# Kernel tuning notes

Measured on AMD Instinct MI355X. Metric: run time of the kernel, lower is better.

## Reference

```python
import jax, jax.numpy as jnp
import numpy as np
import math

# ---- constants lifted verbatim from the torch source ----
PMLX = 10; PX = 400; TX = PMLX + PX + PMLX          # txsize = 420
PMLY = 10; PY = 400; TY = PMLY + PY + PMLY          # tysize = 420
CX = TX // 2; CY = TY // 2
EPS0 = 1e-9 / 36 / math.pi
MU0 = 4 * math.pi * 1e-7
C0 = 1.0 / math.sqrt(MU0 * EPS0)
DX = 2.5e-8; DY = 2.5e-8
DT = 0.99 / C0 / math.sqrt((1.0 / DX) ** 2 + (1.0 / DY) ** 2)
EPSR_INF = 5.283
EPS_INF = EPS0 * EPSR_INF
F0 = 5.47e14; BW = 0.1 * F0
T = math.sqrt(2.0) * math.sqrt(math.log(2.0)) / (math.pi * BW)
NSTEPS = 200   # reduced from 16000 for the correctness baseline; same per-step math


def setup_inputs() -> dict:
    # Lorentz (complex-pole) silver model from param(): pole/residue -> a0,a1,b0,b1,b2
    pr, pi_ = -4.8113e12, 6.8512e13
    rr, ri = 4.9581e14, -1.511e18
    a0 = -2.0 * (pr * rr + pi_ * ri)
    a1 = 2.0 * rr
    b0 = pr * pr + pi_ * pi_
    b1 = -2.0 * pr
    b2 = 1.0
    den = b0 * DT * DT + 2 * b1 * DT + 4 * b2
    Ca = np.array([-(2 * b0 * DT * DT - 8 * b2) / den], np.float32)
    Cb = np.array([-(b0 * DT * DT - 2 * b1 * DT + 4 * b2) / den], np.float32)
    Cc = np.array([(2 * a0 * EPS0 * DT + 4 * a1 * EPS0) / den], np.float32)
    Cd = np.array([-(8 * a1 * EPS0) / den], np.float32)
    Ce = np.array([(-2 * a0 * EPS0 * DT + 4 * a1 * EPS0) / den], np.float32)
    temp1 = float(Cc[0])                       # sum over tot_pol = 1 pole
    denom = EPS_INF / DT + 0.5 * temp1
    C1 = np.full((TX + 1, TY + 1), (EPS_INF / DT) / denom, np.float32)
    C2 = np.full((TX + 1, TY + 1), 0.5 / denom, np.float32)
    Cb_dx = np.full((TX + 1, TY + 1), 1.0 / denom / DX, np.float32)
    Cb_dy = np.full((TX + 1, TY + 1), 1.0 / denom / DY, np.float32)
    dbhx = np.full((TX + 1, TY), DT / MU0 / DY, np.float32)   # Hx curl coeff
    dbhy = np.full((TX, TY + 1), DT / MU0 / DX, np.float32)   # Hy curl coeff
    # polynomial-graded PML conductivity profiles (pml_param)
    m = 4
    eta0 = 120.0 * math.pi
    smax = 0.8 * (m + 1) / (eta0 * DX)

    def prof(n, npml, off):
        k = np.arange(n, dtype=np.float64)
        dl = np.clip(npml - k - off, 0.0, None) / npml   # depth into left PML
        dr = np.clip(k + off - (n - 1 - npml), 0.0, None) / npml
        return (smax * (dl ** m + dr ** m)).astype(np.float32)

    sig_ex = prof(TX + 1, PMLX, 0.0)
    sig_ey = prof(TY + 1, PMLY, 0.0)
    sig_hx = prof(TX, PMLX, 0.5)   # H nodes on half-grid
    sig_hy = prof(TY, PMLY, 0.5)
    # Gaussian-modulated sine soft source at the grid center
    t = np.arange(NSTEPS, dtype=np.float64) * DT
    src = (np.exp(-(((t - 4 * T) / T) ** 2)) * np.sin(2 * math.pi * F0 * (t - 4 * T))).astype(np.float32)
    return {
        "src": jnp.asarray(src), "C1": jnp.asarray(C1), "C2": jnp.asarray(C2),
        "Cb_dx": jnp.asarray(Cb_dx), "Cb_dy": jnp.asarray(Cb_dy),
        "dbhx": jnp.asarray(dbhx), "dbhy": jnp.asarray(dbhy),
        "Ca": jnp.asarray(Ca), "Cb": jnp.asarray(Cb), "Cc": jnp.asarray(Cc),
        "Cd": jnp.asarray(Cd), "Ce": jnp.asarray(Ce),
        "sig_ex": jnp.asarray(sig_ex), "sig_ey": jnp.asarray(sig_ey),
        "sig_hx": jnp.asarray(sig_hx), "sig_hy": jnp.asarray(sig_hy),
        "n_steps": NSTEPS,
    }


def reference(src, C1, C2, Cb_dx, Cb_dy, dbhx, dbhy, Ca, Cb, Cc, Cd, Ce,
              sig_ex, sig_ey, sig_hx, sig_hy, n_steps):
    # PML damping factors (exponential time-stepping of the conductive loss)
    de = jnp.exp(-(sig_ex[:, None] + sig_ey[None, :]) * (DT / EPS0))     # (421,421) for Ez
    dhx = jnp.exp(-(sig_ex[:, None] + sig_hy[None, :]) * (DT / MU0))     # (421,420) for Hx
    dhy = jnp.exp(-(sig_hx[:, None] + sig_ey[None, :]) * (DT / MU0))     # (420,421) for Hy
    # PEC outer boundary mask
    mask = jnp.pad(jnp.ones((TX - 1, TY - 1), de.dtype), ((1, 1), (1, 1)))
    ca = Ca[:, None, None]; cb = Cb[:, None, None]; cc = Cc[:, None, None]
    cd = Cd[:, None, None]; ce = Ce[:, None, None]

    def step(carry, s):
        Ez, Eold, Hx, Hy, Jz, Jold = carry
        # H-field Yee updates with PML damping
        Hx = dhx * (Hx - dbhx * (Ez[:, 1:] - Ez[:, :-1]))
        Hy = dhy * (Hy + dbhy * (Ez[1:, :] - Ez[:-1, :]))
        # curls onto Ez nodes (interior), zero-padded at PEC boundary
        curlHy = jnp.pad(Hy[1:, :] - Hy[:-1, :], ((1, 1), (0, 0)))       # (421,421)
        curlHx = jnp.pad(Hx[:, 1:] - Hx[:, :-1], ((0, 0), (1, 1)))       # (421,421)
        # Lorentz ADE dispersion source term (tot_pol summed; Cc*Ez^{n+1} folded into C1/C2/Cb_*)
        Phi = jnp.sum((ca + 1.0) * Jz + cb * Jold + cd * Ez[None] + ce * Eold[None], axis=0)
        Ez_new = mask * de * (C1 * Ez + Cb_dx * curlHy - Cb_dy * curlHx - C2 * Phi)
        Ez_new = Ez_new.at[CX, CY].add(s)                                 # soft point source
        # polarization current recurrence
        Jz_new = ca * Jz + cb * Jold + cc * Ez_new[None] + cd * Ez[None] + ce * Eold[None]
        return (Ez_new, Ez, Hx, Hy, Jz_new, Jz), None

    z = jnp.zeros((TX + 1, TY + 1), src.dtype)
    init = (z, z,
            jnp.zeros((TX + 1, TY), src.dtype),
            jnp.zeros((TX, TY + 1), src.dtype),
            jnp.zeros((1, TX + 1, TY + 1), src.dtype),
            jnp.zeros((1, TX + 1, TY + 1), src.dtype))
    (Ez, _, _, _, _, _), _ = jax.lax.scan(step, init, src[:n_steps])
    return Ez
```

## Files before the change

### kernel.cpp

```cpp
#include <hip/hip_runtime.h>
#include <math.h>

#define NXr 421
#define CXr 210
#define NSTEPS_C 200

#define Bt   16
#define Kt   8
#define EXT  32
#define SPITCH 34
#define NBLK 27
#define NPHASE (NSTEPS_C / Kt)

#define PP   448
#define PAD  8
#define CP   (CXr + PAD)
#define FSZ  (PP * PP)

struct PParams {
    float *aEz, *aEo, *aJz, *aJo, *aHx, *aHy;
    float *bEz, *bEo, *bJz, *bJo, *bHx, *bHy;
    const float *dexP, *deyP, *aexP, *aeyP, *ahxP, *ahyP;
    const float *C1a, *C2a, *Cbdxa, *Cbdya;
    const float *Caa, *Cba, *Cca, *Cda, *Cea, *dbhxa, *dbhya;
    const float *src;
};

__global__ void init_kernel(const float* __restrict__ sig_ex,
                            const float* __restrict__ sig_ey,
                            const float* __restrict__ sig_hx,
                            const float* __restrict__ sig_hy,
                            float de_fac, float dh_fac,
                            float* __restrict__ zero_base, int n_zero,
                            float* __restrict__ dexP, float* __restrict__ deyP,
                            float* __restrict__ aexP, float* __restrict__ aeyP,
                            float* __restrict__ ahxP, float* __restrict__ ahyP)
{
    int t = blockIdx.x * blockDim.x + threadIdx.x;
    int stride = gridDim.x * blockDim.x;
    for (int k = t; k < n_zero; k += stride) zero_base[k] = 0.0f;
    if (t < PP) {
        int g = t - PAD;
        dexP[t] = (g >= 1 && g <= NXr - 2) ? expf(-sig_ex[g] * de_fac) : 0.0f;
        deyP[t] = (g >= 1 && g <= NXr - 2) ? expf(-sig_ey[g] * de_fac) : 0.0f;
        aexP[t] = (g >= 0 && g <  NXr)     ? expf(-sig_ex[g] * dh_fac) : 0.0f;
        aeyP[t] = (g >= 0 && g <  NXr)     ? expf(-sig_ey[g] * dh_fac) : 0.0f;
        ahxP[t] = (g >= 0 && g <  NXr - 1) ? expf(-sig_hx[g] * dh_fac) : 0.0f;
        ahyP[t] = (g >= 0 && g <  NXr - 1) ? expf(-sig_hy[g] * dh_fac) : 0.0f;
    }
}

__global__ __launch_bounds__(256)
void phase_kernel(PParams p, int t, int bx0, int by0)
{
    __shared__ __align__(16) float sEz[2][EXT][SPITCH];

    const int tid = threadIdx.x;
    const int tj = tid & 15, ti = tid >> 4;
    const int li0 = 2 * ti, lj0 = 2 * tj;
    const int r0 = ((int)blockIdx.x + bx0) * Bt + li0;
    const int c0 = ((int)blockIdx.y + by0) * Bt + lj0;

    const float ca = p.Caa[0], cb = p.Cba[0], cc = p.Cca[0];
    const float cd = p.Cda[0], ce = p.Cea[0];
    const float ca1 = ca + 1.0f;
    const float C1 = p.C1a[0], C2 = p.C2a[0];
    const float cbdx = p.Cbdxa[0], cbdy = p.Cbdya[0];
    const float dbhx0 = p.dbhxa[0], dbhy0 = p.dbhya[0];

    float dHx[2][2], dHy[2][2], dE[2][2], dHyU[2], dHxL[2];
    bool isSrc[2][2];
#pragma unroll
    for (int a = 0; a < 2; ++a)
#pragma unroll
        for (int b = 0; b < 2; ++b) {
            dHx[a][b] = p.aexP[r0 + a] * p.ahyP[c0 + b];
            dHy[a][b] = p.ahxP[r0 + a] * p.aeyP[c0 + b];
            dE[a][b]  = p.dexP[r0 + a] * p.deyP[c0 + b];
            isSrc[a][b] = (r0 + a == CP) && (c0 + b == CP);
        }
    {
        float ahxU = (r0 > 0) ? p.ahxP[r0 - 1] : 0.0f;
        float ahyL = (c0 > 0) ? p.ahyP[c0 - 1] : 0.0f;
        dHyU[0] = ahxU * p.aeyP[c0];
        dHyU[1] = ahxU * p.aeyP[c0 + 1];
        dHxL[0] = p.aexP[r0] * ahyL;
        dHxL[1] = p.aexP[r0 + 1] * ahyL;
    }

    const bool odd = (t & 1) != 0;
    const float* cEz = odd ? p.bEz : p.aEz;
    const float* cEo = odd ? p.bEo : p.aEo;
    const float* cJz = odd ? p.bJz : p.aJz;
    const float* cJo = odd ? p.bJo : p.aJo;
    const float* cHx = odd ? p.bHx : p.aHx;
    const float* cHy = odd ? p.bHy : p.aHy;
    float* nEz = odd ? p.aEz : p.bEz;
    float* nEo = odd ? p.aEo : p.bEo;
    float* nJz = odd ? p.aJz : p.bJz;
    float* nJo = odd ? p.aJo : p.bJo;
    float* nHx = odd ? p.aHx : p.bHx;
    float* nHy = odd ? p.aHy : p.bHy;

    float ez[2][2], eo[2][2], jz[2][2], jo[2][2], hx[2][2], hy[2][2];
#pragma unroll
    for (int a = 0; a < 2; ++a) {
        int g = (r0 + a) * PP + c0;
        float2 v;
        v = *(const float2*)&cEz[g]; ez[a][0] = v.x; ez[a][1] = v.y;
        v = *(const float2*)&cEo[g]; eo[a][0] = v.x; eo[a][1] = v.y;
        v = *(const float2*)&cJz[g]; jz[a][0] = v.x; jz[a][1] = v.y;
        v = *(const float2*)&cJo[g]; jo[a][0] = v.x; jo[a][1] = v.y;
        v = *(const float2*)&cHx[g]; hx[a][0] = v.x; hx[a][1] = v.y;
        v = *(const float2*)&cHy[g]; hy[a][0] = v.x; hy[a][1] = v.y;
    }
    float hyU[2], hxL[2];
    {
        float2 v = *(const float2*)&cHy[(r0 - 1) * PP + c0];
        hyU[0] = v.x; hyU[1] = v.y;
        hxL[0] = cHx[r0 * PP + c0 - 1];
        hxL[1] = cHx[(r0 + 1) * PP + c0 - 1];
    }

    const bool edgeR = (tj == 15), edgeD = (ti == 15);
    const bool edgeU = (ti == 0),  edgeL = (tj == 0);
    const int n0 = t * Kt;

    for (int s = 0; s < Kt; ++s) {
        float (*S)[SPITCH] = sEz[s & 1];
        *(float2*)&S[li0][lj0]     = make_float2(ez[0][0], ez[0][1]);
        *(float2*)&S[li0 + 1][lj0] = make_float2(ez[1][0], ez[1][1]);
        __syncthreads();

        float eR0 = edgeR ? 0.0f : S[li0][lj0 + 2];
        float eR1 = edgeR ? 0.0f : S[li0 + 1][lj0 + 2];
        float2 eD  = edgeD ? make_float2(0.0f, 0.0f)
                           : *(float2*)&S[li0 + 2][lj0];
        float2 eU  = edgeU ? make_float2(0.0f, 0.0f)
                           : *(float2*)&S[li0 - 1][lj0];
        float eL0 = edgeL ? 0.0f : S[li0][lj0 - 1];
        float eL1 = edgeL ? 0.0f : S[li0 + 1][lj0 - 1];

        hx[0][0] = dHx[0][0] * (hx[0][0] - dbhx0 * (ez[0][1] - ez[0][0]));
        hx[0][1] = dHx[0][1] * (hx[0][1] - dbhx0 * (eR0     - ez[0][1]));
        hx[1][0] = dHx[1][0] * (hx[1][0] - dbhx0 * (ez[1][1] - ez[1][0]));
        hx[1][1] = dHx[1][1] * (hx[1][1] - dbhx0 * (eR1     - ez[1][1]));

        hy[0][0] = dHy[0][0] * (hy[0][0] + dbhy0 * (ez[1][0] - ez[0][0]));
        hy[0][1] = dHy[0][1] * (hy[0][1] + dbhy0 * (ez[1][1] - ez[0][1]));
        hy[1][0] = dHy[1][0] * (hy[1][0] + dbhy0 * (eD.x     - ez[1][0]));
        hy[1][1] = dHy[1][1] * (hy[1][1] + dbhy0 * (eD.y     - ez[1][1]));

        hyU[0] = dHyU[0] * (hyU[0] + dbhy0 * (ez[0][0] - eU.x));
        hyU[1] = dHyU[1] * (hyU[1] + dbhy0 * (ez[0][1] - eU.y));
        hxL[0] = dHxL[0] * (hxL[0] - dbhx0 * (ez[0][0] - eL0));
        hxL[1] = dHxL[1] * (hxL[1] - dbhx0 * (ez[1][0] - eL1));

        float sv = p.src[n0 + s];
        float cHyv[2][2], cHxv[2][2];
        cHyv[0][0] = hy[0][0] - hyU[0];   cHxv[0][0] = hx[0][0] - hxL[0];
        cHyv[0][1] = hy[0][1] - hyU[1];   cHxv[0][1] = hx[0][1] - hx[0][0];
        cHyv[1][0] = hy[1][0] - hy[0][0]; cHxv[1][0] = hx[1][0] - hxL[1];
        cHyv[1][1] = hy[1][1] - hy[0][1]; cHxv[1][1] = hx[1][1] - hx[1][0];

#pragma unroll
        for (int a = 0; a < 2; ++a)
#pragma unroll
            for (int b = 0; b < 2; ++b) {
                float e = ez[a][b], eold = eo[a][b];
                float j = jz[a][b], jold = jo[a][b];
                float phi = ca1 * j + cb * jold + cd * e + ce * eold;
                float en = dE[a][b] *
                    (C1 * e + cbdx * cHyv[a][b] - cbdy * cHxv[a][b] - C2 * phi);
                if (isSrc[a][b]) en += sv;
                float jn = phi - j + cc * en;
                eo[a][b] = e;  ez[a][b] = en;
                jo[a][b] = j;  jz[a][b] = jn;
            }
    }

    if (ti >= 4 && ti < 12 && tj >= 4 && tj < 12) {
#pragma unroll
        for (int a = 0; a < 2; ++a) {
            int g = (r0 + a) * PP + c0;
            *(float2*)&nEz[g] = make_float2(ez[a][0], ez[a][1]);
            *(float2*)&nEo[g] = make_float2(eo[a][0], eo[a][1]);
            *(float2*)&nJz[g] = make_float2(jz[a][0], jz[a][1]);
            *(float2*)&nJo[g] = make_float2(jo[a][0], jo[a][1]);
            *(float2*)&nHx[g] = make_float2(hx[a][0], hx[a][1]);
            *(float2*)&nHy[g] = make_float2(hy[a][0], hy[a][1]);
        }
    }
}

__global__ void copy_out_kernel(const float* __restrict__ ezP,
                                float* __restrict__ out)
{
    int idx = blockIdx.x * blockDim.x + threadIdx.x;
    if (idx >= NXr * NXr) return;
    int gi = idx / NXr, gj = idx - gi * NXr;
    out[idx] = ezP[(gi + PAD) * PP + (gj + PAD)];
}

extern "C" void kernel_launch(void* const* d_in, const int* in_sizes, int n_in,
                              void* d_out, int out_size, void* d_ws, size_t ws_size,
                              hipStream_t stream)
{
    const float* src    = (const float*)d_in[0];
    const float* C1     = (const float*)d_in[1];
    const float* C2     = (const float*)d_in[2];
    const float* Cb_dx  = (const float*)d_in[3];
    const float* Cb_dy  = (const float*)d_in[4];
    const float* dbhx   = (const float*)d_in[5];
    const float* dbhy   = (const float*)d_in[6];
    const float* Ca     = (const float*)d_in[7];
    const float* Cb     = (const float*)d_in[8];
    const float* Cc     = (const float*)d_in[9];
    const float* Cd     = (const float*)d_in[10];
    const float* Ce     = (const float*)d_in[11];
    const float* sig_ex = (const float*)d_in[12];
    const float* sig_ey = (const float*)d_in[13];
    const float* sig_hx = (const float*)d_in[14];
    const float* sig_hy = (const float*)d_in[15];

    const double EPS0 = 1e-9 / 36.0 / M_PI;
    const double MU0  = 4.0 * M_PI * 1e-7;
    const double C0   = 1.0 / sqrt(MU0 * EPS0);
    const double DXd  = 2.5e-8, DYd = 2.5e-8;
    const double DT   = 0.99 / C0 / sqrt(1.0 / (DXd * DXd) + 1.0 / (DYd * DYd));
    const float de_fac = (float)(DT / EPS0);
    const float dh_fac = (float)(DT / MU0);

    float* base = (float*)d_ws;
    float* fields = base + PP;
    float* w = fields + 12 * (size_t)FSZ;
    float* dexP = w; w += PP;
    float* deyP = w; w += PP;
    float* aexP = w; w += PP;
    float* aeyP = w; w += PP;
    float* ahxP = w; w += PP;
    float* ahyP = w; w += PP;

    PParams p;
    p.aEz = fields + 0 * (size_t)FSZ;  p.aEo = fields + 1 * (size_t)FSZ;
    p.aJz = fields + 2 * (size_t)FSZ;  p.aJo = fields + 3 * (size_t)FSZ;
    p.aHx = fields + 4 * (size_t)FSZ;  p.aHy = fields + 5 * (size_t)FSZ;
    p.bEz = fields + 6 * (size_t)FSZ;  p.bEo = fields + 7 * (size_t)FSZ;
    p.bJz = fields + 8 * (size_t)FSZ;  p.bJo = fields + 9 * (size_t)FSZ;
    p.bHx = fields + 10 * (size_t)FSZ; p.bHy = fields + 11 * (size_t)FSZ;
    p.dexP = dexP; p.deyP = deyP; p.aexP = aexP; p.aeyP = aeyP;
    p.ahxP = ahxP; p.ahyP = ahyP;
    p.C1a = C1; p.C2a = C2; p.Cbdxa = Cb_dx; p.Cbdya = Cb_dy;
    p.Caa = Ca; p.Cba = Cb; p.Cca = Cc; p.Cda = Cd; p.Cea = Ce;
    p.dbhxa = dbhx; p.dbhya = dbhy;
    p.src = src;

    init_kernel<<<512, 256, 0, stream>>>(sig_ex, sig_ey, sig_hx, sig_hy,
                                         de_fac, dh_fac,
                                         base, PP + 12 * FSZ,
                                         dexP, deyP, aexP, aeyP, ahxP, ahyP);

    dim3 blk(256);
    for (int t = 0; t < NPHASE; ++t) {
        int r  = 8 * t + 12;
        int lo = CP - r, hi = CP + r;
        int b0 = (lo - (EXT - 1)) / 16; if (b0 < 0) b0 = 0;
        int b1 = hi / 16;               if (b1 > NBLK - 1) b1 = NBLK - 1;
        dim3 g(b1 - b0 + 1, b1 - b0 + 1);
        phase_kernel<<<g, blk, 0, stream>>>(p, t, b0, b0);
    }

    copy_out_kernel<<<(NXr * NXr + 255) / 256, 256, 0, stream>>>(p.bEz,
                                                                 (float*)d_out);
}
```

Before: 299.3 us.

## Deepen temporal blocking to 20 steps with 4x4 per-thread register tiles

Raises the temporal-blocking depth from 8 to 20 steps per launch and grows each thread's register tile from 2x2 to 4x4 cells, so each block covers a 64x64 extended tile and writes out a 24x24 core. This cuts the number of phase launches from 25 to 10 and the global traffic per timestep. Coefficients are now formed on the fly from per-row and per-column factors, and the padding and workspace layout change to match. In exchange each block spends more redundant halo work (a 64-wide region for 24 useful cells) and registers per thread go up, which the launch bound of 2 blocks per SM tries to contain.

```diff
diff --git a/kernel.cpp b/kernel.cpp
--- a/kernel.cpp
+++ b/kernel.cpp
@@ -5,15 +5,15 @@
 #define CXr 210
 #define NSTEPS_C 200
 
-#define Bt   16
-#define Kt   8
-#define EXT  32
-#define SPITCH 34
-#define NBLK 27
+#define Bt   24
+#define Kt   20
+#define EXT  64
+#define SPITCH 66
+#define NBLK 18
 #define NPHASE (NSTEPS_C / Kt)
 
-#define PP   448
-#define PAD  8
+#define PP   480
+#define PAD  24
 #define CP   (CXr + PAD)
 #define FSZ  (PP * PP)
 
@@ -50,16 +50,16 @@
     }
 }
 
-__global__ __launch_bounds__(256)
-void phase_kernel(PParams p, int t, int bx0, int by0)
+__global__ __launch_bounds__(256, 2)
+void phase_kernel(PParams p, int t, int b0)
 {
     __shared__ __align__(16) float sEz[2][EXT][SPITCH];
 
     const int tid = threadIdx.x;
     const int tj = tid & 15, ti = tid >> 4;
-    const int li0 = 2 * ti, lj0 = 2 * tj;
-    const int r0 = ((int)blockIdx.x + bx0) * Bt + li0;
-    const int c0 = ((int)blockIdx.y + by0) * Bt + lj0;
+    const int li0 = 4 * ti, lj0 = 4 * tj;
+    const int r0 = ((int)blockIdx.x + b0) * Bt + (PAD - Kt) + li0;
+    const int c0 = ((int)blockIdx.y + b0) * Bt + (PAD - Kt) + lj0;
 
     const float ca = p.Caa[0], cb = p.Cba[0], cc = p.Cca[0];
     const float cd = p.Cda[0], ce = p.Cea[0];
@@ -68,25 +68,18 @@
     const float cbdx = p.Cbdxa[0], cbdy = p.Cbdya[0];
     const float dbhx0 = p.dbhxa[0], dbhy0 = p.dbhya[0];
 
-    float dHx[2][2], dHy[2][2], dE[2][2], dHyU[2], dHxL[2];
-    bool isSrc[2][2];
-#pragma unroll
-    for (int a = 0; a < 2; ++a)
-#pragma unroll
-        for (int b = 0; b < 2; ++b) {
-            dHx[a][b] = p.aexP[r0 + a] * p.ahyP[c0 + b];
-            dHy[a][b] = p.ahxP[r0 + a] * p.aeyP[c0 + b];
-            dE[a][b]  = p.dexP[r0 + a] * p.deyP[c0 + b];
-            isSrc[a][b] = (r0 + a == CP) && (c0 + b == CP);
-        }
-    {
-        float ahxU = (r0 > 0) ? p.ahxP[r0 - 1] : 0.0f;
-        float ahyL = (c0 > 0) ? p.ahyP[c0 - 1] : 0.0f;
-        dHyU[0] = ahxU * p.aeyP[c0];
-        dHyU[1] = ahxU * p.aeyP[c0 + 1];
-        dHxL[0] = p.aexP[r0] * ahyL;
-        dHxL[1] = p.aexP[r0 + 1] * ahyL;
-    }
+    float aexr[4], ahxr[4], dexr[4], aeyc[4], ahyc[4], deyc[4];
+#pragma unroll
+    for (int a = 0; a < 4; ++a) {
+        aexr[a] = p.aexP[r0 + a];
+        ahxr[a] = p.ahxP[r0 + a];
+        dexr[a] = p.dexP[r0 + a];
+        aeyc[a] = p.aeyP[c0 + a];
+        ahyc[a] = p.ahyP[c0 + a];
+        deyc[a] = p.deyP[c0 + a];
+    }
+    const float ahxU = p.ahxP[r0 - 1];
+    const float ahyL = p.ahyP[c0 - 1];
 
     const bool odd = (t & 1) != 0;
     const float* cEz = odd ? p.bEz : p.aEz;
@@ -102,24 +95,24 @@
     float* nHx = odd ? p.aHx : p.bHx;
     float* nHy = odd ? p.aHy : p.bHy;
 
-    float ez[2][2], eo[2][2], jz[2][2], jo[2][2], hx[2][2], hy[2][2];
-#pragma unroll
-    for (int a = 0; a < 2; ++a) {
+    float ez[4][4], eo[4][4], jz[4][4], jo[4][4], hx[4][4], hy[4][4];
+#pragma unroll
+    for (int a = 0; a < 4; ++a) {
         int g = (r0 + a) * PP + c0;
-        float2 v;
-        v = *(const float2*)&cEz[g]; ez[a][0] = v.x; ez[a][1] = v.y;
-        v = *(const float2*)&cEo[g]; eo[a][0] = v.x; eo[a][1] = v.y;
-        v = *(const float2*)&cJz[g]; jz[a][0] = v.x; jz[a][1] = v.y;
-        v = *(const float2*)&cJo[g]; jo[a][0] = v.x; jo[a][1] = v.y;
-        v = *(const float2*)&cHx[g]; hx[a][0] = v.x; hx[a][1] = v.y;
-        v = *(const float2*)&cHy[g]; hy[a][0] = v.x; hy[a][1] = v.y;
-    }
-    float hyU[2], hxL[2];
+        float4 v;
+        v = *(const float4*)&cEz[g]; ez[a][0]=v.x; ez[a][1]=v.y; ez[a][2]=v.z; ez[a][3]=v.w;
+        v = *(const float4*)&cEo[g]; eo[a][0]=v.x; eo[a][1]=v.y; eo[a][2]=v.z; eo[a][3]=v.w;
+        v = *(const float4*)&cJz[g]; jz[a][0]=v.x; jz[a][1]=v.y; jz[a][2]=v.z; jz[a][3]=v.w;
+        v = *(const float4*)&cJo[g]; jo[a][0]=v.x; jo[a][1]=v.y; jo[a][2]=v.z; jo[a][3]=v.w;
+        v = *(const float4*)&cHx[g]; hx[a][0]=v.x; hx[a][1]=v.y; hx[a][2]=v.z; hx[a][3]=v.w;
+        v = *(const float4*)&cHy[g]; hy[a][0]=v.x; hy[a][1]=v.y; hy[a][2]=v.z; hy[a][3]=v.w;
+    }
+    float hyU[4], hxL[4];
     {
-        float2 v = *(const float2*)&cHy[(r0 - 1) * PP + c0];
-        hyU[0] = v.x; hyU[1] = v.y;
-        hxL[0] = cHx[r0 * PP + c0 - 1];
-        hxL[1] = cHx[(r0 + 1) * PP + c0 - 1];
+        float4 v = *(const float4*)&cHy[(r0 - 1) * PP + c0];
+        hyU[0]=v.x; hyU[1]=v.y; hyU[2]=v.z; hyU[3]=v.w;
+#pragma unroll
+        for (int a = 0; a < 4; ++a) hxL[a] = cHx[(r0 + a) * PP + c0 - 1];
     }
 
     const bool edgeR = (tj == 15), edgeD = (ti == 15);
@@ -128,67 +121,80 @@
 
     for (int s = 0; s < Kt; ++s) {
         float (*S)[SPITCH] = sEz[s & 1];
-        *(float2*)&S[li0][lj0]     = make_float2(ez[0][0], ez[0][1]);
-        *(float2*)&S[li0 + 1][lj0] = make_float2(ez[1][0], ez[1][1]);
+#pragma unroll
+        for (int a = 0; a < 4; ++a)
+            *(float4*)&S[li0 + a][lj0] =
+                make_float4(ez[a][0], ez[a][1], ez[a][2], ez[a][3]);
         __syncthreads();
 
-        float eR0 = edgeR ? 0.0f : S[li0][lj0 + 2];
-        float eR1 = edgeR ? 0.0f : S[li0 + 1][lj0 + 2];
-        float2 eD  = edgeD ? make_float2(0.0f, 0.0f)
-                           : *(float2*)&S[li0 + 2][lj0];
-        float2 eU  = edgeU ? make_float2(0.0f, 0.0f)
-                           : *(float2*)&S[li0 - 1][lj0];
-        float eL0 = edgeL ? 0.0f : S[li0][lj0 - 1];
-        float eL1 = edgeL ? 0.0f : S[li0 + 1][lj0 - 1];
-
-        hx[0][0] = dHx[0][0] * (hx[0][0] - dbhx0 * (ez[0][1] - ez[0][0]));
-        hx[0][1] = dHx[0][1] * (hx[0][1] - dbhx0 * (eR0     - ez[0][1]));
-        hx[1][0] = dHx[1][0] * (hx[1][0] - dbhx0 * (ez[1][1] - ez[1][0]));
-        hx[1][1] = dHx[1][1] * (hx[1][1] - dbhx0 * (eR1     - ez[1][1]));
-
-        hy[0][0] = dHy[0][0] * (hy[0][0] + dbhy0 * (ez[1][0] - ez[0][0]));
-        hy[0][1] = dHy[0][1] * (hy[0][1] + dbhy0 * (ez[1][1] - ez[0][1]));
-        hy[1][0] = dHy[1][0] * (hy[1][0] + dbhy0 * (eD.x     - ez[1][0]));
-        hy[1][1] = dHy[1][1] * (hy[1][1] + dbhy0 * (eD.y     - ez[1][1]));
-
-        hyU[0] = dHyU[0] * (hyU[0] + dbhy0 * (ez[0][0] - eU.x));
-        hyU[1] = dHyU[1] * (hyU[1] + dbhy0 * (ez[0][1] - eU.y));
-        hxL[0] = dHxL[0] * (hxL[0] - dbhx0 * (ez[0][0] - eL0));
-        hxL[1] = dHxL[1] * (hxL[1] - dbhx0 * (ez[1][0] - eL1));
+        float eR[4], eL[4];
+#pragma unroll
+        for (int a = 0; a < 4; ++a) {
+            eR[a] = edgeR ? 0.0f : S[li0 + a][lj0 + 4];
+            eL[a] = edgeL ? 0.0f : S[li0 + a][lj0 - 1];
+        }
+        float4 eD4 = edgeD ? make_float4(0.f,0.f,0.f,0.f)
+                           : *(float4*)&S[li0 + 4][lj0];
+        float4 eU4 = edgeU ? make_float4(0.f,0.f,0.f,0.f)
+                           : *(float4*)&S[li0 - 1][lj0];
+        float eD[4] = {eD4.x, eD4.y, eD4.z, eD4.w};
+        float eU[4] = {eU4.x, eU4.y, eU4.z, eU4.w};
+
+#pragma unroll
+        for (int a = 0; a < 4; ++a) {
+#pragma unroll
+            for (int b = 0; b < 3; ++b)
+                hx[a][b] = aexr[a] * ahyc[b] *
+                           (hx[a][b] - dbhx0 * (ez[a][b + 1] - ez[a][b]));
+            hx[a][3] = aexr[a] * ahyc[3] *
+                       (hx[a][3] - dbhx0 * (eR[a] - ez[a][3]));
+        }
+#pragma unroll
+        for (int b = 0; b < 4; ++b) {
+#pragma unroll
+            for (int a = 0; a < 3; ++a)
+                hy[a][b] = ahxr[a] * aeyc[b] *
+                           (hy[a][b] + dbhy0 * (ez[a + 1][b] - ez[a][b]));
+            hy[3][b] = ahxr[3] * aeyc[b] *
+                       (hy[3][b] + dbhy0 * (eD[b] - ez[3][b]));
+        }
+
+#pragma unroll
+        for (int b = 0; b < 4; ++b)
+            hyU[b] = ahxU * aeyc[b] * (hyU[b] + dbhy0 * (ez[0][b] - eU[b]));
+#pragma unroll
+        for (int a = 0; a < 4; ++a)
+            hxL[a] = aexr[a] * ahyL * (hxL[a] - dbhx0 * (ez[a][0] - eL[a]));
 
         float sv = p.src[n0 + s];
-        float cHyv[2][2], cHxv[2][2];
-        cHyv[0][0] = hy[0][0] - hyU[0];   cHxv[0][0] = hx[0][0] - hxL[0];
-        cHyv[0][1] = hy[0][1] - hyU[1];   cHxv[0][1] = hx[0][1] - hx[0][0];
-        cHyv[1][0] = hy[1][0] - hy[0][0]; cHxv[1][0] = hx[1][0] - hxL[1];
-        cHyv[1][1] = hy[1][1] - hy[0][1]; cHxv[1][1] = hx[1][1] - hx[1][0];
-
-#pragma unroll
-        for (int a = 0; a < 2; ++a)
-#pragma unroll
-            for (int b = 0; b < 2; ++b) {
+#pragma unroll
+        for (int a = 0; a < 4; ++a)
+#pragma unroll
+            for (int b = 0; b < 4; ++b) {
+                float cHyv = hy[a][b] - (a ? hy[a - 1][b] : hyU[b]);
+                float cHxv = hx[a][b] - (b ? hx[a][b - 1] : hxL[a]);
                 float e = ez[a][b], eold = eo[a][b];
                 float j = jz[a][b], jold = jo[a][b];
                 float phi = ca1 * j + cb * jold + cd * e + ce * eold;
-                float en = dE[a][b] *
-                    (C1 * e + cbdx * cHyv[a][b] - cbdy * cHxv[a][b] - C2 * phi);
-                if (isSrc[a][b]) en += sv;
+                float en = (dexr[a] * deyc[b]) *
+                    (C1 * e + cbdx * cHyv - cbdy * cHxv - C2 * phi);
+                if (r0 + a == CP && c0 + b == CP) en += sv;
                 float jn = phi - j + cc * en;
                 eo[a][b] = e;  ez[a][b] = en;
                 jo[a][b] = j;  jz[a][b] = jn;
             }
     }
 
-    if (ti >= 4 && ti < 12 && tj >= 4 && tj < 12) {
-#pragma unroll
-        for (int a = 0; a < 2; ++a) {
+    if (ti >= 5 && ti < 11 && tj >= 5 && tj < 11) {
+#pragma unroll
+        for (int a = 0; a < 4; ++a) {
             int g = (r0 + a) * PP + c0;
-            *(float2*)&nEz[g] = make_float2(ez[a][0], ez[a][1]);
-            *(float2*)&nEo[g] = make_float2(eo[a][0], eo[a][1]);
-            *(float2*)&nJz[g] = make_float2(jz[a][0], jz[a][1]);
-            *(float2*)&nJo[g] = make_float2(jo[a][0], jo[a][1]);
-            *(float2*)&nHx[g] = make_float2(hx[a][0], hx[a][1]);
-            *(float2*)&nHy[g] = make_float2(hy[a][0], hy[a][1]);
+            *(float4*)&nEz[g] = make_float4(ez[a][0], ez[a][1], ez[a][2], ez[a][3]);
+            *(float4*)&nEo[g] = make_float4(eo[a][0], eo[a][1], eo[a][2], eo[a][3]);
+            *(float4*)&nJz[g] = make_float4(jz[a][0], jz[a][1], jz[a][2], jz[a][3]);
+            *(float4*)&nJo[g] = make_float4(jo[a][0], jo[a][1], jo[a][2], jo[a][3]);
+            *(float4*)&nHx[g] = make_float4(hx[a][0], hx[a][1], hx[a][2], hx[a][3]);
+            *(float4*)&nHy[g] = make_float4(hy[a][0], hy[a][1], hy[a][2], hy[a][3]);
         }
     }
 }
@@ -231,8 +237,7 @@
     const float de_fac = (float)(DT / EPS0);
     const float dh_fac = (float)(DT / MU0);
 
-    float* base = (float*)d_ws;
-    float* fields = base + PP;
+    float* fields = (float*)d_ws;
     float* w = fields + 12 * (size_t)FSZ;
     float* dexP = w; w += PP;
     float* deyP = w; w += PP;
@@ -257,19 +262,19 @@
 
     init_kernel<<<512, 256, 0, stream>>>(sig_ex, sig_ey, sig_hx, sig_hy,
                                          de_fac, dh_fac,
-                                         base, PP + 12 * FSZ,
+                                         fields, 12 * FSZ,
                                          dexP, deyP, aexP, aeyP, ahxP, ahyP);
 
     dim3 blk(256);
     for (int t = 0; t < NPHASE; ++t) {
-        int r  = 8 * t + 12;
+        int r  = 20 * t + 24;
         int lo = CP - r, hi = CP + r;
-        int b0 = (lo - (EXT - 1)) / 16; if (b0 < 0) b0 = 0;
-        int b1 = hi / 16;               if (b1 > NBLK - 1) b1 = NBLK - 1;
+        int b0 = (lo - 68) / Bt; if (b0 < 0) b0 = 0;
+        int b1 = (hi - 4) / Bt;  if (b1 > NBLK - 1) b1 = NBLK - 1;
         dim3 g(b1 - b0 + 1, b1 - b0 + 1);
-        phase_kernel<<<g, blk, 0, stream>>>(p, t, b0, b0);
-    }
-
-    copy_out_kernel<<<(NXr * NXr + 255) / 256, 256, 0, stream>>>(p.bEz,
+        phase_kernel<<<g, blk, 0, stream>>>(p, t, b0);
+    }
+
+    copy_out_kernel<<<(NXr * NXr + 255) / 256, 256, 0, stream>>>(p.aEz,
                                                                  (float*)d_out);
 }
```

Result: slower. 373.5 us (+24.8%).
